# Kernel optimization log

Measured on AMD Instinct MI355X. Metric: run time of the kernel, lower is better.

## Reference

```python
import jax, jax.numpy as jnp
import numpy as np

H = 16  # num_heads
D = 64  # head_dim


def setup_inputs() -> dict:
    key = jax.random.key(0)
    k1, k2, k3, k4 = jax.random.split(key, 4)
    x = jax.random.normal(k1, (4, 4096, 512), dtype=jnp.float32)
    w_in = jax.random.normal(k2, (1024, 512), dtype=jnp.float32) * 0.02
    w_qkv = jax.random.normal(k3, (3072, 1024), dtype=jnp.float32) * 0.02
    w_out = jax.random.normal(k4, (1024, 1024), dtype=jnp.float32) * 0.02
    norm_w = jnp.ones((1024,), dtype=jnp.float32)
    return {"x": x, "w_in": w_in, "w_qkv": w_qkv, "w_out": w_out, "norm_w": norm_w}


def reference(x, w_in, w_qkv, w_out, norm_w):
    B, L, _ = x.shape
    x_proj = jnp.einsum('bli,di->bld', x, w_in)  # (B,L,latent)
    qkv = jnp.einsum('bld,ed->ble', x_proj, w_qkv).reshape(B, L, 3, H, D)
    qkv = jnp.transpose(qkv, (2, 0, 3, 1, 4))  # (3,B,H,L,D)
    q, k, v = qkv[0], qkv[1], qkv[2]
    if L <= 64:
        scale = D ** (-0.5)
        attn = jnp.einsum('bhld,bhmd->bhlm', q, k) * scale
        attn = jax.nn.softmax(attn.astype(jnp.float32), axis=-1).astype(q.dtype)
        out = jnp.einsum('bhlm,bhmd->bhld', attn, v)
    else:
        qf = jax.nn.elu(q) + 1.0
        kf = jax.nn.elu(k) + 1.0
        kv = jnp.einsum('bhld,bhlm->bhdm', kf, v)        # (B,H,D,D)
        out = jnp.einsum('bhld,bhdm->bhlm', qf, kv)      # (B,H,L,D)
        k_sum = jnp.sum(kf, axis=2, keepdims=True)        # (B,H,1,D)
        normalizer = jnp.einsum('bhld,bhmd->bhlm', qf, k_sum)  # (B,H,L,1)
        out = out / (normalizer + 1e-8)
    # NOTE: faithful to torch source — raw reshape of (B,H,L,D) -> (B,L,H*D)
    out = out.reshape(B, L, H * D)
    out = jnp.einsum('bld,ed->ble', out, w_out)
    y = out + x_proj
    eps = jnp.finfo(jnp.float32).eps
    rms = jax.lax.rsqrt(jnp.mean(y * y, axis=-1, keepdims=True) + eps)
    return y * rms * norm_w
```

## Files before the change

kernel.cpp:

```cpp
#include <hip/hip_runtime.h>
#include <stdint.h>

typedef unsigned short u16;
typedef unsigned int u32;

typedef __bf16 bf16_t;
typedef bf16_t bf16x8 __attribute__((ext_vector_type(8)));
typedef float f32x4 __attribute__((ext_vector_type(4)));

__device__ __forceinline__ u16 f2b(float f) {
    u32 u = __builtin_bit_cast(u32, f);
    u += 0x7FFFu + ((u >> 16) & 1u);
    return (u16)(u >> 16);
}
__device__ __forceinline__ float b2f(u16 h) {
    return __builtin_bit_cast(float, (u32)h << 16);
}

__device__ __forceinline__ void gld_lds16(const void* gptr, void* lptr) {
    __builtin_amdgcn_global_load_lds(
        (const __attribute__((address_space(1))) void*)gptr,
        (__attribute__((address_space(3))) void*)lptr,
        16, 0, 0);
}

__global__ __launch_bounds__(256) void cvt_kernel(const float* __restrict__ s,
                                                  u16* __restrict__ d, int n4) {
    int i = blockIdx.x * 256 + threadIdx.x;
    const int stride = gridDim.x * 256;
    for (; i < n4; i += stride) {
        float4 v = reinterpret_cast<const float4*>(s)[i];
        uint2 o;
        o.x = (u32)f2b(v.x) | ((u32)f2b(v.y) << 16);
        o.y = (u32)f2b(v.z) | ((u32)f2b(v.w) << 16);
        reinterpret_cast<uint2*>(d)[i] = o;
    }
}

template <int EPI>
__global__ __launch_bounds__(256) void gemm_bt(
    const u16* __restrict__ A, const u16* __restrict__ Bw,
    float* __restrict__ outF, u16* __restrict__ outB,
    const u16* __restrict__ residB, int N, int K)
{
    __shared__ u16 As[8192];
    __shared__ u16 Bs[8192];

    const int t = threadIdx.x;
    const int ntile = N >> 7;
    const int mt = blockIdx.x / ntile;
    const int nt = blockIdx.x - mt * ntile;
    const size_t brow = (size_t)mt << 7;
    const size_t bcol = (size_t)nt << 7;

    const int lane = t & 63;
    const int wv = t >> 6;
    const int wrow = (wv >> 1) << 6;
    const int wcol = (wv & 1) << 6;
    const int fr = lane & 15;
    const int fk = lane >> 4;
    const int swz = (fr & 7) << 4;

    f32x4 acc[4][4] = {};

    const int srow = t >> 3;
    const int pb = (t & 7) << 4;

    for (int k0 = 0; k0 < K; k0 += 64) {
#pragma unroll
        for (int i = 0; i < 4; ++i) {
            const int row = (i << 5) + srow;
            const int kb = pb ^ ((row & 7) << 4);
            const u16* ga = A + (brow + row) * (size_t)K + (k0 + (kb >> 1));
            const u16* gb = Bw + (bcol + row) * (size_t)K + (k0 + (kb >> 1));
            gld_lds16(ga, As + (i << 11) + t * 8);
            gld_lds16(gb, Bs + (i << 11) + t * 8);
        }
        __syncthreads();
#pragma unroll
        for (int ks = 0; ks < 2; ++ks) {
            const int col = ((ks << 6) | (fk << 4)) ^ swz;
            bf16x8 af[4], bfr[4];
#pragma unroll
            for (int i = 0; i < 4; ++i) {
                af[i]  = *(const bf16x8*)((const char*)As + (wrow + (i << 4) + fr) * 128 + col);
                bfr[i] = *(const bf16x8*)((const char*)Bs + (wcol + (i << 4) + fr) * 128 + col);
            }
#pragma unroll
            for (int i = 0; i < 4; ++i)
#pragma unroll
                for (int j = 0; j < 4; ++j)
                    acc[i][j] = __builtin_amdgcn_mfma_f32_16x16x32_bf16(
                        af[i], bfr[j], acc[i][j], 0, 0, 0);
        }
        __syncthreads();
    }

    const int r0 = (lane >> 4) << 2;
    const int c0 = lane & 15;
#pragma unroll
    for (int i = 0; i < 4; ++i) {
#pragma unroll
        for (int r = 0; r < 4; ++r) {
            const size_t grow = brow + wrow + (i << 4) + r0 + r;
#pragma unroll
            for (int j = 0; j < 4; ++j) {
                const size_t gcol = bcol + wcol + (j << 4) + c0;
                float v = acc[i][j][r];
                const size_t idx = grow * (size_t)N + gcol;
                if (EPI == 0) {
                    outB[idx] = f2b(v);
                } else if (EPI == 1) {
                    if (gcol < 2048) v = (v > 0.f) ? (v + 1.f) : __expf(v);
                    outB[idx] = f2b(v);
                } else {
                    outF[idx] = v + b2f(residB[idx]);
                }
            }
        }
    }
}

__global__ __launch_bounds__(256) void attn_kv(
    const u16* __restrict__ qkvb, float* __restrict__ kvpart, float* __restrict__ kspart)
{
    __shared__ __align__(16) u16 kfs[2048];
    __shared__ __align__(16) u16 vss[2048];
    __shared__ float ksp[4][64];
    const int t = threadIdx.x;
    const int bh = blockIdx.x >> 3;
    const int split = blockIdx.x & 7;
    const int b = bh >> 4, h = bh & 15;
    const size_t base = (size_t)b * (4096 * 3072) + h * 64;
    const int wv = t >> 6, lane = t & 63;
    const int lload = t >> 3, dload = (t & 7) << 3;
    const int dg = t >> 5;
    const int m0 = (t & 31) << 1;

    float acc[8][2] = {};
    float ks = 0.f;

    for (int c = 0; c < 512; c += 32) {
        __syncthreads();
        const size_t l = (size_t)split * 512 + c + lload;
        *(uint4*)(kfs + lload * 64 + dload) = *(const uint4*)(qkvb + base + l * 3072 + 1024 + dload);
        *(uint4*)(vss + lload * 64 + dload) = *(const uint4*)(qkvb + base + l * 3072 + 2048 + dload);
        __syncthreads();
#pragma unroll 4
        for (int ll = 0; ll < 32; ++ll) {
            const uint4 kfu = *(const uint4*)(kfs + ll * 64 + (dg << 3));
            const u32 vu = *(const u32*)(vss + ll * 64 + m0);
            const float v0 = __builtin_bit_cast(float, vu << 16);
            const float v1 = __builtin_bit_cast(float, vu & 0xFFFF0000u);
            const u32 kw[4] = {kfu.x, kfu.y, kfu.z, kfu.w};
#pragma unroll
            for (int p = 0; p < 4; ++p) {
                const float klo = __builtin_bit_cast(float, kw[p] << 16);
                const float khi = __builtin_bit_cast(float, kw[p] & 0xFFFF0000u);
                acc[2 * p][0]     += klo * v0;
                acc[2 * p][1]     += klo * v1;
                acc[2 * p + 1][0] += khi * v0;
                acc[2 * p + 1][1] += khi * v1;
            }
        }
        const int lb = wv << 3;
#pragma unroll
        for (int q = 0; q < 8; ++q) ks += b2f(kfs[(lb + q) * 64 + lane]);
    }
    ksp[wv][lane] = ks;
    const size_t obase = (size_t)blockIdx.x * 4096;
#pragma unroll
    for (int i = 0; i < 8; ++i) {
        float2 w = {acc[i][0], acc[i][1]};
        *(float2*)(kvpart + obase + (size_t)((dg << 3) + i) * 64 + m0) = w;
    }
    __syncthreads();
    if (t < 64)
        kspart[(size_t)blockIdx.x * 64 + t] = ksp[0][t] + ksp[1][t] + ksp[2][t] + ksp[3][t];
}

__global__ __launch_bounds__(256) void attn_red(
    const float* __restrict__ kvpart, const float* __restrict__ kspart,
    u16* __restrict__ kvtb)
{
    const int bh = blockIdx.x;
    const int t = threadIdx.x;
    const size_t pbase = (size_t)bh * 8 * 4096;
    u16* ob = kvtb + (size_t)bh * 6144;
#pragma unroll 2
    for (int rep = 0; rep < 16; ++rep) {
        const int e = rep * 256 + t;
        float s = 0.f;
#pragma unroll
        for (int p = 0; p < 8; ++p) s += kvpart[pbase + (size_t)p * 4096 + e];
        const int d = e >> 6, m = e & 63;
        ob[m * 64 + d] = f2b(s);
    }
    if (t < 64) {
        float s = 0.f;
#pragma unroll
        for (int p = 0; p < 8; ++p) s += kspart[(size_t)(bh * 8 + p) * 64 + t];
        ob[64 * 64 + t] = f2b(s);
    }
    for (int z = t; z < 1984; z += 256) ob[65 * 64 + z] = 0;
}

__global__ __launch_bounds__(256) void attn_out_mfma(
    const u16* __restrict__ qkvb, const u16* __restrict__ kvtb,
    u16* __restrict__ attnb)
{
    __shared__ u16 As[8192];
    __shared__ u16 Bs[6144];
    const int t = threadIdx.x;
    const int bh = blockIdx.x >> 5;
    const int lt = blockIdx.x & 31;
    const int b = bh >> 4, h = bh & 15;
    const size_t qbase = (size_t)b * (4096 * 3072) + h * 64;
    const int l0 = lt << 7;

    const int lane = t & 63;
    const int wv = t >> 6;
    const int fr = lane & 15;
    const int fk = lane >> 4;
    const int swz = (fr & 7) << 4;
    const int srow = t >> 3;
    const int pb = (t & 7) << 4;

#pragma unroll
    for (int i = 0; i < 4; ++i) {
        const int row = (i << 5) + srow;
        const int kb = pb ^ ((row & 7) << 4);
        gld_lds16(qkvb + qbase + (size_t)(l0 + row) * 3072 + (kb >> 1),
                  As + (i << 11) + t * 8);
    }
#pragma unroll
    for (int i = 0; i < 3; ++i) {
        const int row = (i << 5) + srow;
        const int kb = pb ^ ((row & 7) << 4);
        gld_lds16(kvtb + (size_t)bh * 6144 + row * 64 + (kb >> 1),
                  Bs + (i << 11) + t * 8);
    }
    __syncthreads();

    f32x4 acc[2][5] = {};
    const int wrow = wv << 5;
#pragma unroll
    for (int ks = 0; ks < 2; ++ks) {
        const int col = ((ks << 6) | (fk << 4)) ^ swz;
        bf16x8 af[2], bfr[5];
#pragma unroll
        for (int i = 0; i < 2; ++i)
            af[i] = *(const bf16x8*)((const char*)As + (wrow + (i << 4) + fr) * 128 + col);
#pragma unroll
        for (int j = 0; j < 5; ++j)
            bfr[j] = *(const bf16x8*)((const char*)Bs + ((j << 4) + fr) * 128 + col);
#pragma unroll
        for (int i = 0; i < 2; ++i)
#pragma unroll
            for (int j = 0; j < 5; ++j)
                acc[i][j] = __builtin_amdgcn_mfma_f32_16x16x32_bf16(
                    af[i], bfr[j], acc[i][j], 0, 0, 0);
    }

    const int r0 = (lane >> 4) << 2;
    const int c0 = lane & 15;
#pragma unroll
    for (int i = 0; i < 2; ++i) {
#pragma unroll
        for (int r = 0; r < 4; ++r) {
            const int row = wrow + (i << 4) + r0 + r;
            const float nv = __shfl(acc[i][4][r], lane & 48, 64);
            const float inv = 1.f / (nv + 1e-8f);
            const size_t obase = ((size_t)bh * 4096 + l0 + row) * 64;
#pragma unroll
            for (int j = 0; j < 4; ++j)
                attnb[obase + (j << 4) + c0] = f2b(acc[i][j][r] * inv);
        }
    }
}

__global__ __launch_bounds__(256) void rms_kernel(float* __restrict__ y,
                                                  const float* __restrict__ nw)
{
    __shared__ float red[4];
    const size_t row = blockIdx.x;
    const int t = threadIdx.x;
    float4 v = *(float4*)(y + row * 1024 + t * 4);
    float s = v.x * v.x + v.y * v.y + v.z * v.z + v.w * v.w;
#pragma unroll
    for (int off = 32; off > 0; off >>= 1) s += __shfl_down(s, off, 64);
    if ((t & 63) == 0) red[t >> 6] = s;
    __syncthreads();
    const float tot = red[0] + red[1] + red[2] + red[3];
    const float rms = rsqrtf(tot * (1.f / 1024.f) + 1.1920929e-7f);
    const float4 w = *(const float4*)(nw + t * 4);
    v.x *= rms * w.x; v.y *= rms * w.y; v.z *= rms * w.z; v.w *= rms * w.w;
    *(float4*)(y + row * 1024 + t * 4) = v;
}

extern "C" void kernel_launch(void* const* d_in, const int* in_sizes, int n_in,
                              void* d_out, int out_size, void* d_ws, size_t ws_size,
                              hipStream_t stream)
{
    const float* x     = (const float*)d_in[0];
    const float* w_in  = (const float*)d_in[1];
    const float* w_qkv = (const float*)d_in[2];
    const float* w_out = (const float*)d_in[3];
    const float* normw = (const float*)d_in[4];
    float* out = (float*)d_out;

    char* ws = (char*)d_ws;
    size_t off = 0;
    auto alloc = [&](size_t bytes) {
        char* p = ws + off;
        off += (bytes + 255) & ~(size_t)255;
        return p;
    };
    u16* xb    = (u16*)alloc(8388608ull * 2);
    u16* wib   = (u16*)alloc(524288ull * 2);
    u16* wqb   = (u16*)alloc(3145728ull * 2);
    u16* wob   = (u16*)alloc(1048576ull * 2);
    u16* xpb   = (u16*)alloc(16777216ull * 2);
    u16* qkvb  = (u16*)alloc(50331648ull * 2);
    float* kvp = (float*)alloc(512ull * 4096 * 4);
    float* ksp = (float*)alloc(512ull * 64 * 4);
    u16* kvtb  = (u16*)alloc(64ull * 96 * 64 * 2);
    u16* attnb = (u16*)alloc(16777216ull * 2);

    cvt_kernel<<<2048, 256, 0, stream>>>(x, xb, 8388608 / 4);
    cvt_kernel<<<512, 256, 0, stream>>>(w_in, wib, 524288 / 4);
    cvt_kernel<<<1024, 256, 0, stream>>>(w_qkv, wqb, 3145728 / 4);
    cvt_kernel<<<1024, 256, 0, stream>>>(w_out, wob, 1048576 / 4);

    gemm_bt<0><<<1024, 256, 0, stream>>>(xb, wib, nullptr, xpb, nullptr, 1024, 512);
    gemm_bt<1><<<3072, 256, 0, stream>>>(xpb, wqb, nullptr, qkvb, nullptr, 3072, 1024);

    attn_kv<<<512, 256, 0, stream>>>(qkvb, kvp, ksp);
    attn_red<<<64, 256, 0, stream>>>(kvp, ksp, kvtb);
    attn_out_mfma<<<2048, 256, 0, stream>>>(qkvb, kvtb, attnb);

    gemm_bt<2><<<1024, 256, 0, stream>>>(attnb, wob, out, nullptr, xpb, 1024, 1024);
    rms_kernel<<<16384, 256, 0, stream>>>(out, normw);
}
```

Baseline: 435.0 us.

## Replace 128x128 GEMM with 256x256 double-buffered pipelined 8-wave kernel

Replaces the single-buffered 128x128-tile GEMM with a 256x256-tile, 512-thread kernel. It double-buffers LDS and interleaves async global-to-LDS loads for the next k-tiles with MFMA quadrant phases, using explicit vmcnt gates and s_setprio. It also remaps workgroup IDs so neighbouring workgroups touch nearby tiles, aiming for better L2 locality. The intent is to raise arithmetic intensity per tile and hide load latency behind compute. In exchange it uses far more LDS per block (128 KB) and more registers, which lowers occupancy and leaves fewer workgroups to fill the CUs.

```diff
diff --git a/kernel.cpp b/kernel.cpp
--- a/kernel.cpp
+++ b/kernel.cpp
@@ -37,76 +37,105 @@
     }
 }
 
+#define PHASE(c, qm, qn, STAGES, GATE) do {                                    \
+    bf16x8 af[4][2]; bf16x8 bfv[2][2];                                         \
+    _Pragma("unroll") for (int ii = 0; ii < 4; ++ii) {                         \
+        const int r = (qm)*128 + wm*64 + ii*16 + fr;                           \
+        const char* pa = (const char*)AS[c] + r*128; const int rs = (r&7)<<4;  \
+        af[ii][0] = *(const bf16x8*)(pa + ((fk<<4)^rs));                       \
+        af[ii][1] = *(const bf16x8*)(pa + ((64|(fk<<4))^rs)); }                \
+    _Pragma("unroll") for (int jj = 0; jj < 2; ++jj) {                         \
+        const int r = (qn)*128 + wn*32 + jj*16 + fr;                           \
+        const char* pb = (const char*)BS[c] + r*128; const int rs = (r&7)<<4;  \
+        bfv[jj][0] = *(const bf16x8*)(pb + ((fk<<4)^rs));                      \
+        bfv[jj][1] = *(const bf16x8*)(pb + ((64|(fk<<4))^rs)); }               \
+    STAGES;                                                                    \
+    __builtin_amdgcn_s_barrier();                                              \
+    __builtin_amdgcn_s_setprio(1);                                             \
+    _Pragma("unroll") for (int ks = 0; ks < 2; ++ks)                           \
+      _Pragma("unroll") for (int ii = 0; ii < 4; ++ii)                         \
+        _Pragma("unroll") for (int jj = 0; jj < 2; ++jj)                       \
+            acc[(qm)*4+ii][(qn)*2+jj] = __builtin_amdgcn_mfma_f32_16x16x32_bf16( \
+                af[ii][ks], bfv[jj][ks], acc[(qm)*4+ii][(qn)*2+jj], 0, 0, 0);  \
+    __builtin_amdgcn_s_setprio(0);                                             \
+    GATE;                                                                      \
+    __builtin_amdgcn_s_barrier();                                              \
+} while (0)
+
+#define VGATE asm volatile("s_waitcnt vmcnt(4)" ::: "memory")
+#define NOGATE ((void)0)
+
 template <int EPI>
-__global__ __launch_bounds__(256) void gemm_bt(
+__global__ __launch_bounds__(512) void gemm_bt256(
     const u16* __restrict__ A, const u16* __restrict__ Bw,
     float* __restrict__ outF, u16* __restrict__ outB,
     const u16* __restrict__ residB, int N, int K)
 {
-    __shared__ u16 As[8192];
-    __shared__ u16 Bs[8192];
-
-    const int t = threadIdx.x;
-    const int ntile = N >> 7;
-    const int mt = blockIdx.x / ntile;
-    const int nt = blockIdx.x - mt * ntile;
-    const size_t brow = (size_t)mt << 7;
-    const size_t bcol = (size_t)nt << 7;
-
-    const int lane = t & 63;
-    const int wv = t >> 6;
-    const int wrow = (wv >> 1) << 6;
-    const int wcol = (wv & 1) << 6;
-    const int fr = lane & 15;
-    const int fk = lane >> 4;
-    const int swz = (fr & 7) << 4;
-
-    f32x4 acc[4][4] = {};
-
-    const int srow = t >> 3;
-    const int pb = (t & 7) << 4;
-
-    for (int k0 = 0; k0 < K; k0 += 64) {
-#pragma unroll
-        for (int i = 0; i < 4; ++i) {
-            const int row = (i << 5) + srow;
-            const int kb = pb ^ ((row & 7) << 4);
-            const u16* ga = A + (brow + row) * (size_t)K + (k0 + (kb >> 1));
-            const u16* gb = Bw + (bcol + row) * (size_t)K + (k0 + (kb >> 1));
-            gld_lds16(ga, As + (i << 11) + t * 8);
-            gld_lds16(gb, Bs + (i << 11) + t * 8);
+    __shared__ u16 AS[2][16384];
+    __shared__ u16 BS[2][16384];
+
+    const int t = threadIdx.x;
+    const int ntile = N >> 8;
+    const int nwg = gridDim.x;
+    const int wg = ((int)blockIdx.x & 7) * (nwg >> 3) + ((int)blockIdx.x >> 3);
+    const int mt = wg / ntile;
+    const int nt = wg - mt * ntile;
+    const size_t brow = (size_t)mt << 8;
+    const size_t bcol = (size_t)nt << 8;
+
+    const int lane = t & 63, wv = t >> 6;
+    const int wm = wv >> 2, wn = wv & 3;
+    const int fr = lane & 15, fk = lane >> 4;
+    const int nkt = K >> 6;
+    const int niter = nkt >> 1;
+
+    f32x4 acc[8][4] = {};
+
+    auto STG = [&](int c, int half, int isA, int kt) {
+        const u16* G = isA ? A : Bw;
+        const size_t g0 = isA ? brow : bcol;
+        u16* lds = isA ? AS[c] : BS[c];
+        const int k0 = kt << 6;
+#pragma unroll
+        for (int j = 0; j < 2; ++j) {
+            const int row = (half << 7) + (j << 6) + (t >> 3);
+            const int kb = ((t & 7) << 4) ^ ((row & 7) << 4);
+            gld_lds16(G + (g0 + row) * (size_t)K + k0 + (kb >> 1),
+                      lds + row * 64 + (t & 7) * 8);
         }
-        __syncthreads();
-#pragma unroll
-        for (int ks = 0; ks < 2; ++ks) {
-            const int col = ((ks << 6) | (fk << 4)) ^ swz;
-            bf16x8 af[4], bfr[4];
-#pragma unroll
-            for (int i = 0; i < 4; ++i) {
-                af[i]  = *(const bf16x8*)((const char*)As + (wrow + (i << 4) + fr) * 128 + col);
-                bfr[i] = *(const bf16x8*)((const char*)Bs + (wcol + (i << 4) + fr) * 128 + col);
-            }
-#pragma unroll
-            for (int i = 0; i < 4; ++i)
-#pragma unroll
-                for (int j = 0; j < 4; ++j)
-                    acc[i][j] = __builtin_amdgcn_mfma_f32_16x16x32_bf16(
-                        af[i], bfr[j], acc[i][j], 0, 0, 0);
-        }
-        __syncthreads();
+    };
+
+    STG(0, 0, 1, 0); STG(0, 1, 1, 0); STG(0, 0, 0, 0); STG(0, 1, 0, 0);
+    STG(1, 0, 1, 1); STG(1, 1, 0, 1);
+    asm volatile("s_waitcnt vmcnt(4)" ::: "memory");
+    __builtin_amdgcn_s_barrier();
+
+#pragma unroll 1
+    for (int i = 0; i < niter; ++i) {
+        const int kt1 = 2 * i + 1, kt2 = 2 * i + 2, kt3 = 2 * i + 3;
+        const bool more = kt2 < nkt;
+        PHASE(0, 0, 0, STG(1, 1, 1, kt1), NOGATE);
+        PHASE(0, 0, 1, STG(1, 0, 0, kt1), NOGATE);
+        PHASE(0, 1, 1, if (more) STG(0, 0, 1, kt2), NOGATE);
+        PHASE(0, 1, 0, if (more) STG(0, 1, 0, kt2), VGATE);
+        PHASE(1, 0, 0, if (more) STG(0, 1, 1, kt2), NOGATE);
+        PHASE(1, 0, 1, if (more) STG(0, 0, 0, kt2), NOGATE);
+        PHASE(1, 1, 1, if (more) STG(1, 0, 1, kt3), NOGATE);
+        PHASE(1, 1, 0, if (more) STG(1, 1, 0, kt3), VGATE);
     }
 
     const int r0 = (lane >> 4) << 2;
     const int c0 = lane & 15;
 #pragma unroll
-    for (int i = 0; i < 4; ++i) {
+    for (int f = 0; f < 8; ++f) {
+        const size_t growb = brow + ((f >> 2) * 128 + wm * 64 + (f & 3) * 16 + r0);
 #pragma unroll
         for (int r = 0; r < 4; ++r) {
-            const size_t grow = brow + wrow + (i << 4) + r0 + r;
-#pragma unroll
-            for (int j = 0; j < 4; ++j) {
-                const size_t gcol = bcol + wcol + (j << 4) + c0;
-                float v = acc[i][j][r];
+            const size_t grow = growb + r;
+#pragma unroll
+            for (int g = 0; g < 4; ++g) {
+                const size_t gcol = bcol + ((g >> 1) * 128 + wn * 32 + (g & 1) * 16) + c0;
+                float v = acc[f][g][r];
                 const size_t idx = grow * (size_t)N + gcol;
                 if (EPI == 0) {
                     outB[idx] = f2b(v);
@@ -332,13 +361,13 @@
     cvt_kernel<<<1024, 256, 0, stream>>>(w_qkv, wqb, 3145728 / 4);
     cvt_kernel<<<1024, 256, 0, stream>>>(w_out, wob, 1048576 / 4);
 
-    gemm_bt<0><<<1024, 256, 0, stream>>>(xb, wib, nullptr, xpb, nullptr, 1024, 512);
-    gemm_bt<1><<<3072, 256, 0, stream>>>(xpb, wqb, nullptr, qkvb, nullptr, 3072, 1024);
+    gemm_bt256<0><<<256, 512, 0, stream>>>(xb, wib, nullptr, xpb, nullptr, 1024, 512);
+    gemm_bt256<1><<<768, 512, 0, stream>>>(xpb, wqb, nullptr, qkvb, nullptr, 3072, 1024);
 
     attn_kv<<<512, 256, 0, stream>>>(qkvb, kvp, ksp);
     attn_red<<<64, 256, 0, stream>>>(kvp, ksp, kvtb);
     attn_out_mfma<<<2048, 256, 0, stream>>>(qkvb, kvtb, attnb);
 
-    gemm_bt<2><<<1024, 256, 0, stream>>>(attnb, wob, out, nullptr, xpb, 1024, 1024);
+    gemm_bt256<2><<<256, 512, 0, stream>>>(attnb, wob, out, nullptr, xpb, 1024, 1024);
     rms_kernel<<<16384, 256, 0, stream>>>(out, normw);
 }
```

Result: faster. 389.1 us (-10.6%).
